# Optimization experiments

Measured on AMD Instinct MI355X. Metric: run time of the kernel, lower is better.

## Reference

```python
import jax, jax.numpy as jnp
import numpy as np

B, D = 500000, 3
EPS = 1e-8

def _matrix_sqrt_H(A):
    # Hermitian sqrt via eigh: Q diag((L^2)^0.25) Q^T  (matches torch code incl. |L| handling)
    L, Q = jnp.linalg.eigh(A)
    return jnp.einsum('bij,bj,bkj->bik', Q, (L ** 2) ** 0.25, Q)

def setup_inputs() -> dict:
    key = jax.random.key(0)
    k1, k2, k3, k4 = jax.random.split(key, 4)
    miu_1 = jax.random.normal(k1, (B, D), dtype=jnp.float32)
    miu_2 = jax.random.normal(k2, (B, D), dtype=jnp.float32)
    eye = jnp.eye(D, dtype=jnp.float32)
    M1 = jax.random.normal(k3, (B, D, D), dtype=jnp.float32)
    M2 = jax.random.normal(k4, (B, D, D), dtype=jnp.float32)
    # SPD covariances, as produced by a Gaussian-splatting pipeline
    cov_1 = 0.1 * jnp.einsum('bij,bkj->bik', M1, M1) + 1e-3 * eye
    cov_2 = 0.1 * jnp.einsum('bij,bkj->bik', M2, M2) + 1e-3 * eye
    return {"miu_1": miu_1, "miu_2": miu_2, "cov_1": cov_1, "cov_2": cov_2}

def reference(miu_1, miu_2, cov_1, cov_2):
    eye = jnp.eye(cov_1.shape[-1], dtype=cov_1.dtype)
    A_sqrt = _matrix_sqrt_H(cov_1 + eye * EPS)
    A_sqrt_inv = jnp.linalg.inv(A_sqrt + eye * EPS)
    C = jnp.einsum('bij,bjk,blk->bil', A_sqrt, cov_2, A_sqrt)  # A_sqrt cov_2 A_sqrt^T
    C_sqrt = _matrix_sqrt_H(C + eye * EPS)
    cov_velocity = jnp.einsum('bij,bjk,blk->bil', A_sqrt, C_sqrt, A_sqrt_inv)
    cov_velocity = cov_velocity + jnp.swapaxes(cov_velocity, -1, -2) - 2.0 * cov_1
    return (miu_2 - miu_1, cov_velocity)
```

## Files before the change

### kernel.cpp

```cpp
#include <hip/hip_runtime.h>
#include <math.h>

#define EPS 1e-8f

__device__ __forceinline__ void jrot(float A[3][3], float Q[3][3], int p, int q, int r) {
    float apq  = A[p][q];
    float diff = A[q][q] - A[p][p];
    float theta = diff * __builtin_amdgcn_rcpf(2.0f * apq);
    float t = __builtin_amdgcn_rcpf(fabsf(theta) + sqrtf(fmaf(theta, theta, 1.0f)));
    t = copysignf(t, theta);
    t = (fabsf(apq) < 1e-30f) ? 0.0f : t;
    float c = __builtin_amdgcn_rsqf(fmaf(t, t, 1.0f));
    float s = t * c;
    float tapq = t * apq;
    A[p][p] -= tapq;
    A[q][q] += tapq;
    A[p][q] = 0.0f; A[q][p] = 0.0f;
    float arp = A[r][p], arq = A[r][q];
    A[r][p] = fmaf(c, arp, -s * arq); A[p][r] = A[r][p];
    A[r][q] = fmaf(c, arq,  s * arp); A[q][r] = A[r][q];
    #pragma unroll
    for (int i = 0; i < 3; ++i) {
        float qip = Q[i][p], qiq = Q[i][q];
        Q[i][p] = fmaf(c, qip, -s * qiq);
        Q[i][q] = fmaf(s, qip,  c * qiq);
    }
}

__device__ __forceinline__ void eigh3f(float A[3][3], float Q[3][3]) {
    Q[0][0] = 1.0f; Q[0][1] = 0.0f; Q[0][2] = 0.0f;
    Q[1][0] = 0.0f; Q[1][1] = 1.0f; Q[1][2] = 0.0f;
    Q[2][0] = 0.0f; Q[2][1] = 0.0f; Q[2][2] = 1.0f;
    #pragma unroll
    for (int sweep = 0; sweep < 5; ++sweep) {
        jrot(A, Q, 0, 1, 2);
        jrot(A, Q, 0, 2, 1);
        jrot(A, Q, 1, 2, 0);
    }
}

__global__ __launch_bounds__(256) void wasserstein_log_kernel(
    const float* __restrict__ miu1, const float* __restrict__ miu2,
    const float* __restrict__ cov1, const float* __restrict__ cov2,
    float* __restrict__ out, int B)
{
    int b = blockIdx.x * blockDim.x + threadIdx.x;
    if (b >= B) return;

    out[3*b + 0] = miu2[3*b + 0] - miu1[3*b + 0];
    out[3*b + 1] = miu2[3*b + 1] - miu1[3*b + 1];
    out[3*b + 2] = miu2[3*b + 2] - miu1[3*b + 2];

    float c1[3][3], c2m[3][3];
    #pragma unroll
    for (int i = 0; i < 3; ++i)
        #pragma unroll
        for (int j = 0; j < 3; ++j) {
            c1[i][j]  = cov1[9*b + 3*i + j];
            c2m[i][j] = cov2[9*b + 3*i + j];
        }

    float A[3][3];
    #pragma unroll
    for (int i = 0; i < 3; ++i)
        #pragma unroll
        for (int j = 0; j < 3; ++j)
            A[i][j] = c1[i][j] + (i == j ? EPS : 0.0f);
    float Q[3][3];
    eigh3f(A, Q);

    float s[3], si[3];
    #pragma unroll
    for (int k = 0; k < 3; ++k) {
        s[k]  = sqrtf(fabsf(A[k][k]));
        si[k] = __builtin_amdgcn_rcpf(s[k] + EPS);
    }

    float S[3][3], Sinv[3][3];
    #pragma unroll
    for (int i = 0; i < 3; ++i)
        #pragma unroll
        for (int j = 0; j < 3; ++j) {
            S[i][j]    = fmaf(Q[i][0]*s[0],  Q[j][0], fmaf(Q[i][1]*s[1],  Q[j][1], Q[i][2]*s[2]  * Q[j][2]));
            Sinv[i][j] = fmaf(Q[i][0]*si[0], Q[j][0], fmaf(Q[i][1]*si[1], Q[j][1], Q[i][2]*si[2] * Q[j][2]));
        }

    float T[3][3];
    #pragma unroll
    for (int i = 0; i < 3; ++i)
        #pragma unroll
        for (int k = 0; k < 3; ++k)
            T[i][k] = fmaf(S[i][0], c2m[0][k], fmaf(S[i][1], c2m[1][k], S[i][2]*c2m[2][k]));
    float C[3][3];
    #pragma unroll
    for (int i = 0; i < 3; ++i)
        #pragma unroll
        for (int l = 0; l < 3; ++l)
            C[i][l] = fmaf(T[i][0], S[l][0], fmaf(T[i][1], S[l][1], T[i][2]*S[l][2]))
                      + (i == l ? EPS : 0.0f);

    float Qc[3][3];
    eigh3f(C, Qc);
    float t0 = sqrtf(fabsf(C[0][0])), t1 = sqrtf(fabsf(C[1][1])), t2 = sqrtf(fabsf(C[2][2]));
    float Csq[3][3];
    #pragma unroll
    for (int i = 0; i < 3; ++i)
        #pragma unroll
        for (int j = 0; j < 3; ++j)
            Csq[i][j] = fmaf(Qc[i][0]*t0, Qc[j][0], fmaf(Qc[i][1]*t1, Qc[j][1], Qc[i][2]*t2 * Qc[j][2]));

    float T2[3][3];
    #pragma unroll
    for (int i = 0; i < 3; ++i)
        #pragma unroll
        for (int k = 0; k < 3; ++k)
            T2[i][k] = fmaf(S[i][0], Csq[0][k], fmaf(S[i][1], Csq[1][k], S[i][2]*Csq[2][k]));
    float V[3][3];
    #pragma unroll
    for (int i = 0; i < 3; ++i)
        #pragma unroll
        for (int l = 0; l < 3; ++l)
            V[i][l] = fmaf(T2[i][0], Sinv[l][0], fmaf(T2[i][1], Sinv[l][1], T2[i][2]*Sinv[l][2]));

    float* out_cov = out + (size_t)3 * B;
    #pragma unroll
    for (int i = 0; i < 3; ++i)
        #pragma unroll
        for (int j = 0; j < 3; ++j)
            out_cov[9*b + 3*i + j] = V[i][j] + V[j][i] - 2.0f*c1[i][j];
}

extern "C" void kernel_launch(void* const* d_in, const int* in_sizes, int n_in,
                              void* d_out, int out_size, void* d_ws, size_t ws_size,
                              hipStream_t stream) {
    const float* miu1 = (const float*)d_in[0];
    const float* miu2 = (const float*)d_in[1];
    const float* cov1 = (const float*)d_in[2];
    const float* cov2 = (const float*)d_in[3];
    float* out = (float*)d_out;
    int B = in_sizes[0] / 3;
    int threads = 256;
    int blocks = (B + threads - 1) / threads;
    hipLaunchKernelGGL(wasserstein_log_kernel, dim3(blocks), dim3(threads), 0, stream,
                       miu1, miu2, cov1, cov2, out, B);
}
```

Baseline: 108.4 us.

## Work in eigenbasis, cheaper Jacobi rotation, fewer sweeps, two items per thread

Several changes at once. The Jacobi rotation now computes c and s from half-angle formulas using rsq and sqrt instead of the tan formulation, and each eigensolve runs 4 sweeps instead of 5. C is formed directly in A's eigenbasis, so the explicit S and Sinv matrices are no longer built, and the final product is fused into U·diag(tsq)·Pᵀ. Each thread now handles two batch elements, which halves the grid. Together these cut ALU work and instruction count, at the cost of slightly lower Jacobi accuracy and higher register pressure.

```diff
diff --git a/kernel.cpp b/kernel.cpp
--- a/kernel.cpp
+++ b/kernel.cpp
@@ -5,13 +5,18 @@
 
 __device__ __forceinline__ void jrot(float A[3][3], float Q[3][3], int p, int q, int r) {
     float apq  = A[p][q];
-    float diff = A[q][q] - A[p][p];
-    float theta = diff * __builtin_amdgcn_rcpf(2.0f * apq);
-    float t = __builtin_amdgcn_rcpf(fabsf(theta) + sqrtf(fmaf(theta, theta, 1.0f)));
-    t = copysignf(t, theta);
-    t = (fabsf(apq) < 1e-30f) ? 0.0f : t;
-    float c = __builtin_amdgcn_rsqf(fmaf(t, t, 1.0f));
-    float s = t * c;
+    float h    = A[q][q] - A[p][p];
+    float ah   = fabsf(h) + 1e-18f;
+    float v    = apq + apq;
+    float rad  = fmaf(ah, ah, v * v);
+    float rr   = __builtin_amdgcn_rsqf(rad);
+    float c2   = ah * rr;
+    float s2h  = apq * rr;
+    s2h = (h < 0.0f) ? -s2h : s2h;
+    float c    = sqrtf(fmaf(0.5f, c2, 0.5f));
+    float rc   = __builtin_amdgcn_rcpf(c);
+    float s    = s2h * rc;
+    float t    = s * rc;
     float tapq = t * apq;
     A[p][p] -= tapq;
     A[q][q] += tapq;
@@ -32,7 +37,7 @@
     Q[1][0] = 0.0f; Q[1][1] = 1.0f; Q[1][2] = 0.0f;
     Q[2][0] = 0.0f; Q[2][1] = 0.0f; Q[2][2] = 1.0f;
     #pragma unroll
-    for (int sweep = 0; sweep < 5; ++sweep) {
+    for (int sweep = 0; sweep < 4; ++sweep) {
         jrot(A, Q, 0, 1, 2);
         jrot(A, Q, 0, 2, 1);
         jrot(A, Q, 1, 2, 0);
@@ -42,92 +47,95 @@
 __global__ __launch_bounds__(256) void wasserstein_log_kernel(
     const float* __restrict__ miu1, const float* __restrict__ miu2,
     const float* __restrict__ cov1, const float* __restrict__ cov2,
-    float* __restrict__ out, int B)
+    float* __restrict__ out, int B, int B2)
 {
-    int b = blockIdx.x * blockDim.x + threadIdx.x;
-    if (b >= B) return;
+    int b0 = blockIdx.x * blockDim.x + threadIdx.x;
+    if (b0 >= B2) return;
+    float* out_cov = out + (size_t)3 * B;
 
-    out[3*b + 0] = miu2[3*b + 0] - miu1[3*b + 0];
-    out[3*b + 1] = miu2[3*b + 1] - miu1[3*b + 1];
-    out[3*b + 2] = miu2[3*b + 2] - miu1[3*b + 2];
+    #pragma unroll
+    for (int e = 0; e < 2; ++e) {
+        int b = b0 + e * B2;
+        if (b >= B) continue;
 
-    float c1[3][3], c2m[3][3];
-    #pragma unroll
-    for (int i = 0; i < 3; ++i)
+        out[3*b + 0] = miu2[3*b + 0] - miu1[3*b + 0];
+        out[3*b + 1] = miu2[3*b + 1] - miu1[3*b + 1];
+        out[3*b + 2] = miu2[3*b + 2] - miu1[3*b + 2];
+
+        float A[3][3], M[3][3];
         #pragma unroll
-        for (int j = 0; j < 3; ++j) {
-            c1[i][j]  = cov1[9*b + 3*i + j];
-            c2m[i][j] = cov2[9*b + 3*i + j];
+        for (int i = 0; i < 3; ++i)
+            #pragma unroll
+            for (int j = 0; j < 3; ++j) {
+                A[i][j] = cov1[9*b + 3*i + j];
+                M[i][j] = cov2[9*b + 3*i + j];
+            }
+        float k00 = A[0][0], k01 = A[0][1], k02 = A[0][2];
+        float k11 = A[1][1], k12 = A[1][2], k22 = A[2][2];
+        A[0][0] += EPS; A[1][1] += EPS; A[2][2] += EPS;
+
+        float Q[3][3];
+        eigh3f(A, Q);
+
+        float d[3], di[3];
+        #pragma unroll
+        for (int k = 0; k < 3; ++k) {
+            float w = fmaxf(fabsf(A[k][k]), 1e-12f);
+            di[k] = __builtin_amdgcn_rsqf(w);
+            d[k]  = w * di[k];
         }
 
-    float A[3][3];
-    #pragma unroll
-    for (int i = 0; i < 3; ++i)
+        float T[3][3];
         #pragma unroll
-        for (int j = 0; j < 3; ++j)
-            A[i][j] = c1[i][j] + (i == j ? EPS : 0.0f);
-    float Q[3][3];
-    eigh3f(A, Q);
+        for (int i = 0; i < 3; ++i)
+            #pragma unroll
+            for (int j = 0; j < 3; ++j)
+                T[i][j] = fmaf(Q[0][i], M[0][j], fmaf(Q[1][i], M[1][j], Q[2][i]*M[2][j]));
+        float Cp[3][3];
+        #pragma unroll
+        for (int i = 0; i < 3; ++i)
+            #pragma unroll
+            for (int j = 0; j < 3; ++j) {
+                float g = fmaf(T[i][0], Q[0][j], fmaf(T[i][1], Q[1][j], T[i][2]*Q[2][j]));
+                Cp[i][j] = d[i] * d[j] * g + (i == j ? EPS : 0.0f);
+            }
 
-    float s[3], si[3];
-    #pragma unroll
-    for (int k = 0; k < 3; ++k) {
-        s[k]  = sqrtf(fabsf(A[k][k]));
-        si[k] = __builtin_amdgcn_rcpf(s[k] + EPS);
-    }
-
-    float S[3][3], Sinv[3][3];
-    #pragma unroll
-    for (int i = 0; i < 3; ++i)
+        float Qc[3][3];
+        eigh3f(Cp, Qc);
+        float tsq[3];
         #pragma unroll
-        for (int j = 0; j < 3; ++j) {
-            S[i][j]    = fmaf(Q[i][0]*s[0],  Q[j][0], fmaf(Q[i][1]*s[1],  Q[j][1], Q[i][2]*s[2]  * Q[j][2]));
-            Sinv[i][j] = fmaf(Q[i][0]*si[0], Q[j][0], fmaf(Q[i][1]*si[1], Q[j][1], Q[i][2]*si[2] * Q[j][2]));
+        for (int k = 0; k < 3; ++k) {
+            float wc = fmaxf(fabsf(Cp[k][k]), 1e-12f);
+            tsq[k] = wc * __builtin_amdgcn_rsqf(wc);
         }
 
-    float T[3][3];
-    #pragma unroll
-    for (int i = 0; i < 3; ++i)
+        float U[3][3], P[3][3];
         #pragma unroll
-        for (int k = 0; k < 3; ++k)
-            T[i][k] = fmaf(S[i][0], c2m[0][k], fmaf(S[i][1], c2m[1][k], S[i][2]*c2m[2][k]));
-    float C[3][3];
-    #pragma unroll
-    for (int i = 0; i < 3; ++i)
+        for (int i = 0; i < 3; ++i)
+            #pragma unroll
+            for (int j = 0; j < 3; ++j) {
+                float q0 = Q[i][0], q1 = Q[i][1], q2 = Q[i][2];
+                U[i][j] = fmaf(q0*d[0],  Qc[0][j], fmaf(q1*d[1],  Qc[1][j], q2*d[2]  * Qc[2][j]));
+                P[i][j] = fmaf(q0*di[0], Qc[0][j], fmaf(q1*di[1], Qc[1][j], q2*di[2] * Qc[2][j]));
+            }
+        float V[3][3];
         #pragma unroll
-        for (int l = 0; l < 3; ++l)
-            C[i][l] = fmaf(T[i][0], S[l][0], fmaf(T[i][1], S[l][1], T[i][2]*S[l][2]))
-                      + (i == l ? EPS : 0.0f);
+        for (int i = 0; i < 3; ++i)
+            #pragma unroll
+            for (int j = 0; j < 3; ++j)
+                V[i][j] = fmaf(U[i][0]*tsq[0], P[j][0],
+                          fmaf(U[i][1]*tsq[1], P[j][1], U[i][2]*tsq[2] * P[j][2]));
 
-    float Qc[3][3];
-    eigh3f(C, Qc);
-    float t0 = sqrtf(fabsf(C[0][0])), t1 = sqrtf(fabsf(C[1][1])), t2 = sqrtf(fabsf(C[2][2]));
-    float Csq[3][3];
-    #pragma unroll
-    for (int i = 0; i < 3; ++i)
-        #pragma unroll
-        for (int j = 0; j < 3; ++j)
-            Csq[i][j] = fmaf(Qc[i][0]*t0, Qc[j][0], fmaf(Qc[i][1]*t1, Qc[j][1], Qc[i][2]*t2 * Qc[j][2]));
-
-    float T2[3][3];
-    #pragma unroll
-    for (int i = 0; i < 3; ++i)
-        #pragma unroll
-        for (int k = 0; k < 3; ++k)
-            T2[i][k] = fmaf(S[i][0], Csq[0][k], fmaf(S[i][1], Csq[1][k], S[i][2]*Csq[2][k]));
-    float V[3][3];
-    #pragma unroll
-    for (int i = 0; i < 3; ++i)
-        #pragma unroll
-        for (int l = 0; l < 3; ++l)
-            V[i][l] = fmaf(T2[i][0], Sinv[l][0], fmaf(T2[i][1], Sinv[l][1], T2[i][2]*Sinv[l][2]));
-
-    float* out_cov = out + (size_t)3 * B;
-    #pragma unroll
-    for (int i = 0; i < 3; ++i)
-        #pragma unroll
-        for (int j = 0; j < 3; ++j)
-            out_cov[9*b + 3*i + j] = V[i][j] + V[j][i] - 2.0f*c1[i][j];
+        out_cov[9*b + 0] = V[0][0] + V[0][0] - 2.0f*k00;
+        out_cov[9*b + 1] = V[0][1] + V[1][0] - 2.0f*k01;
+        out_cov[9*b + 2] = V[0][2] + V[2][0] - 2.0f*k02;
+        out_cov[9*b + 3] = V[1][0] + V[0][1] - 2.0f*k01;
+        out_cov[9*b + 4] = V[1][1] + V[1][1] - 2.0f*k11;
+        out_cov[9*b + 5] = V[1][2] + V[2][1] - 2.0f*k12;
+        out_cov[9*b + 6] = V[2][0] + V[0][2] - 2.0f*k02;
+        out_cov[9*b + 7] = V[2][1] + V[1][2] - 2.0f*k12;
+        out_cov[9*b + 8] = V[2][2] + V[2][2] - 2.0f*k22;
+    }
 }
 
 extern "C" void kernel_launch(void* const* d_in, const int* in_sizes, int n_in,
@@ -138,9 +146,10 @@
     const float* cov1 = (const float*)d_in[2];
     const float* cov2 = (const float*)d_in[3];
     float* out = (float*)d_out;
-    int B = in_sizes[0] / 3;
+    int B  = in_sizes[0] / 3;
+    int B2 = (B + 1) / 2;
     int threads = 256;
-    int blocks = (B + threads - 1) / threads;
+    int blocks = (B2 + threads - 1) / threads;
     hipLaunchKernelGGL(wasserstein_log_kernel, dim3(blocks), dim3(threads), 0, stream,
-                       miu1, miu2, cov1, cov2, out, B);
+                       miu1, miu2, cov1, cov2, out, B, B2);
 }
```

Result: faster. 105.2 us (-3.0%).

## Process two matrices per thread with packed float2 math and reduced Jacobi sweeps

Applied to the files above, without the earlier changes.

Each thread now handles two batch elements packed as float2 vectors, so the compiler can emit packed FP32 instructions. The Jacobi eigensolver is cut from 5 sweeps to one specialised first sweep plus 2 full sweeps, and the rotation angle is computed with a half-angle rsqrt formula. Loads and stores use 16-byte vector accesses, and only the symmetric half of each matrix is read. The algebra is restructured to reuse eigenvectors of A (C formed in the Q basis) and to build the symmetric output directly. Fewer sweeps may lower accuracy on ill-conditioned matrices, and halving the thread count reduces parallelism.

```diff
diff --git a/kernel.cpp b/kernel.cpp
--- a/kernel.cpp
+++ b/kernel.cpp
@@ -3,131 +3,245 @@
 
 #define EPS 1e-8f
 
-__device__ __forceinline__ void jrot(float A[3][3], float Q[3][3], int p, int q, int r) {
-    float apq  = A[p][q];
-    float diff = A[q][q] - A[p][p];
-    float theta = diff * __builtin_amdgcn_rcpf(2.0f * apq);
-    float t = __builtin_amdgcn_rcpf(fabsf(theta) + sqrtf(fmaf(theta, theta, 1.0f)));
-    t = copysignf(t, theta);
-    t = (fabsf(apq) < 1e-30f) ? 0.0f : t;
-    float c = __builtin_amdgcn_rsqf(fmaf(t, t, 1.0f));
-    float s = t * c;
-    float tapq = t * apq;
-    A[p][p] -= tapq;
-    A[q][q] += tapq;
-    A[p][q] = 0.0f; A[q][p] = 0.0f;
-    float arp = A[r][p], arq = A[r][q];
-    A[r][p] = fmaf(c, arp, -s * arq); A[p][r] = A[r][p];
-    A[r][q] = fmaf(c, arq,  s * arp); A[q][r] = A[r][q];
+typedef float v2  __attribute__((ext_vector_type(2)));
+typedef float f4a __attribute__((ext_vector_type(4), aligned(4)));
+
+static __device__ __forceinline__ v2 vfma(v2 a, v2 b, v2 c) {
+#if __has_builtin(__builtin_elementwise_fma)
+    return __builtin_elementwise_fma(a, b, c);
+#else
+    return a * b + c;
+#endif
+}
+static __device__ __forceinline__ v2 vrsq(v2 x) {
+    v2 r; r.x = __builtin_amdgcn_rsqf(x.x); r.y = __builtin_amdgcn_rsqf(x.y); return r;
+}
+static __device__ __forceinline__ v2 vsq(v2 x)         { return __builtin_elementwise_sqrt(x); }
+static __device__ __forceinline__ v2 vab(v2 x)         { return __builtin_elementwise_abs(x); }
+static __device__ __forceinline__ v2 vmx(v2 a, v2 b)   { return __builtin_elementwise_max(a, b); }
+static __device__ __forceinline__ v2 vcs(v2 a, v2 b)   { return __builtin_elementwise_copysign(a, b); }
+
+static __device__ __forceinline__ void jangle(v2 app, v2 aqq, v2 apq,
+                                              v2 &c, v2 &s, v2 &app2, v2 &aqq2) {
+    v2 h   = aqq - app;
+    v2 ah  = vab(h) + 1e-18f;
+    v2 v   = apq + apq;
+    v2 rad = vfma(ah, ah, v * v);
+    v2 rr  = vrsq(rad);
+    v2 c2  = ah * rr;
+    c = vsq(vfma((v2)0.5f, c2, (v2)0.5f));
+    v2 s2 = vmx(vfma((v2)(-0.5f), c2, (v2)0.5f), (v2)0.0f);
+    s = vcs(vsq(s2), apq * h);
+    v2 dl = vcs(vfma(rad, rr, -ah), h) * 0.5f;
+    app2 = app - dl;
+    aqq2 = aqq + dl;
+}
+
+static __device__ __forceinline__ void eigh3(
+    v2 &a00, v2 &a01, v2 &a02, v2 &a11, v2 &a12, v2 &a22,
+    v2 &q00, v2 &q01, v2 &q02, v2 &q10, v2 &q11, v2 &q12, v2 &q20, v2 &q21, v2 &q22)
+{
+    v2 c, s, x, y, t0, t1;
+    jangle(a00, a11, a01, c, s, x, y); a00 = x; a11 = y; a01 = (v2)0.0f;
+    t0 = a02; t1 = a12; a02 = vfma(c, t0, -s * t1); a12 = vfma(c, t1, s * t0);
+    q00 = c; q01 = s; q10 = -s; q11 = c;
+
+    jangle(a00, a22, a02, c, s, x, y); a00 = x; a22 = y; a02 = (v2)0.0f;
+    t0 = a01; t1 = a12; a01 = vfma(c, t0, -s * t1); a12 = vfma(c, t1, s * t0);
+    q02 = s * q00; q12 = s * q10; q20 = -s; q22 = c;
+    q00 = c * q00; q10 = c * q10;
+
+    jangle(a11, a22, a12, c, s, x, y); a11 = x; a22 = y; a12 = (v2)0.0f;
+    t0 = a01; t1 = a02; a01 = vfma(c, t0, -s * t1); a02 = vfma(c, t1, s * t0);
+    t0 = q01; t1 = q02; q01 = vfma(c, t0, -s * t1); q02 = vfma(s, t0, c * t1);
+    t0 = q11; t1 = q12; q11 = vfma(c, t0, -s * t1); q12 = vfma(s, t0, c * t1);
+    q21 = -s * q22; q22 = c * q22;
+
     #pragma unroll
-    for (int i = 0; i < 3; ++i) {
-        float qip = Q[i][p], qiq = Q[i][q];
-        Q[i][p] = fmaf(c, qip, -s * qiq);
-        Q[i][q] = fmaf(s, qip,  c * qiq);
+    for (int sw = 0; sw < 2; ++sw) {
+        jangle(a00, a11, a01, c, s, x, y); a00 = x; a11 = y; a01 = (v2)0.0f;
+        t0 = a02; t1 = a12; a02 = vfma(c, t0, -s * t1); a12 = vfma(c, t1, s * t0);
+        t0 = q00; t1 = q01; q00 = vfma(c, t0, -s * t1); q01 = vfma(s, t0, c * t1);
+        t0 = q10; t1 = q11; q10 = vfma(c, t0, -s * t1); q11 = vfma(s, t0, c * t1);
+        t0 = q20; t1 = q21; q20 = vfma(c, t0, -s * t1); q21 = vfma(s, t0, c * t1);
+
+        jangle(a00, a22, a02, c, s, x, y); a00 = x; a22 = y; a02 = (v2)0.0f;
+        t0 = a01; t1 = a12; a01 = vfma(c, t0, -s * t1); a12 = vfma(c, t1, s * t0);
+        t0 = q00; t1 = q02; q00 = vfma(c, t0, -s * t1); q02 = vfma(s, t0, c * t1);
+        t0 = q10; t1 = q12; q10 = vfma(c, t0, -s * t1); q12 = vfma(s, t0, c * t1);
+        t0 = q20; t1 = q22; q20 = vfma(c, t0, -s * t1); q22 = vfma(s, t0, c * t1);
+
+        jangle(a11, a22, a12, c, s, x, y); a11 = x; a22 = y; a12 = (v2)0.0f;
+        t0 = a01; t1 = a02; a01 = vfma(c, t0, -s * t1); a02 = vfma(c, t1, s * t0);
+        t0 = q01; t1 = q02; q01 = vfma(c, t0, -s * t1); q02 = vfma(s, t0, c * t1);
+        t0 = q11; t1 = q12; q11 = vfma(c, t0, -s * t1); q12 = vfma(s, t0, c * t1);
+        t0 = q21; t1 = q22; q21 = vfma(c, t0, -s * t1); q22 = vfma(s, t0, c * t1);
     }
 }
 
-__device__ __forceinline__ void eigh3f(float A[3][3], float Q[3][3]) {
-    Q[0][0] = 1.0f; Q[0][1] = 0.0f; Q[0][2] = 0.0f;
-    Q[1][0] = 0.0f; Q[1][1] = 1.0f; Q[1][2] = 0.0f;
-    Q[2][0] = 0.0f; Q[2][1] = 0.0f; Q[2][2] = 1.0f;
-    #pragma unroll
-    for (int sweep = 0; sweep < 5; ++sweep) {
-        jrot(A, Q, 0, 1, 2);
-        jrot(A, Q, 0, 2, 1);
-        jrot(A, Q, 1, 2, 0);
-    }
-}
-
-__global__ __launch_bounds__(256) void wasserstein_log_kernel(
+__global__ __launch_bounds__(256, 4) void wasserstein_log_kernel(
     const float* __restrict__ miu1, const float* __restrict__ miu2,
     const float* __restrict__ cov1, const float* __restrict__ cov2,
     float* __restrict__ out, int B)
 {
-    int b = blockIdx.x * blockDim.x + threadIdx.x;
-    if (b >= B) return;
-
-    out[3*b + 0] = miu2[3*b + 0] - miu1[3*b + 0];
-    out[3*b + 1] = miu2[3*b + 1] - miu1[3*b + 1];
-    out[3*b + 2] = miu2[3*b + 2] - miu1[3*b + 2];
-
-    float c1[3][3], c2m[3][3];
-    #pragma unroll
-    for (int i = 0; i < 3; ++i)
-        #pragma unroll
-        for (int j = 0; j < 3; ++j) {
-            c1[i][j]  = cov1[9*b + 3*i + j];
-            c2m[i][j] = cov2[9*b + 3*i + j];
-        }
-
-    float A[3][3];
-    #pragma unroll
-    for (int i = 0; i < 3; ++i)
-        #pragma unroll
-        for (int j = 0; j < 3; ++j)
-            A[i][j] = c1[i][j] + (i == j ? EPS : 0.0f);
-    float Q[3][3];
-    eigh3f(A, Q);
-
-    float s[3], si[3];
-    #pragma unroll
-    for (int k = 0; k < 3; ++k) {
-        s[k]  = sqrtf(fabsf(A[k][k]));
-        si[k] = __builtin_amdgcn_rcpf(s[k] + EPS);
+    int b0 = blockIdx.x * blockDim.x + threadIdx.x;
+    int nT = (B + 1) >> 1;
+    if (b0 >= nT) return;
+    bool pair = (2 * b0 + 1 < B);
+
+    v2 k00, k01, k02, k11, k12, k22;
+    v2 m00, m01, m02, m11, m12, m22;
+    v2 u0, u1, u2;
+
+    if (pair) {
+        size_t cb = 18 * (size_t)b0;
+        const f4a* p1 = (const f4a*)(cov1 + cb);
+        f4a A0 = p1[0], A1 = p1[1], A2 = p1[2], A3 = p1[3];
+        float a17 = cov1[cb + 17];
+        k00.x = A0.x; k00.y = A2.y;
+        k01.x = A0.y; k01.y = A2.z;
+        k02.x = A0.z; k02.y = A2.w;
+        k11.x = A1.x; k11.y = A3.y;
+        k12.x = A1.y; k12.y = A3.z;
+        k22.x = A2.x; k22.y = a17;
+
+        const f4a* p2 = (const f4a*)(cov2 + cb);
+        f4a B0 = p2[0], B1 = p2[1], B2 = p2[2], B3 = p2[3];
+        float b17 = cov2[cb + 17];
+        m00.x = B0.x; m00.y = B2.y;
+        m01.x = B0.y; m01.y = B2.z;
+        m02.x = B0.z; m02.y = B2.w;
+        m11.x = B1.x; m11.y = B3.y;
+        m12.x = B1.y; m12.y = B3.z;
+        m22.x = B2.x; m22.y = b17;
+
+        size_t mb = 6 * (size_t)b0;
+        const f4a* q1 = (const f4a*)(miu1 + mb);
+        const f4a* q2 = (const f4a*)(miu2 + mb);
+        f4a M1 = q1[0]; float m1a = miu1[mb + 4], m1b = miu1[mb + 5];
+        f4a M2 = q2[0]; float m2a = miu2[mb + 4], m2b = miu2[mb + 5];
+        u0.x = M2.x - M1.x; u0.y = M2.w - M1.w;
+        u1.x = M2.y - M1.y; u1.y = m2a - m1a;
+        u2.x = M2.z - M1.z; u2.y = m2b - m1b;
+    } else {
+        size_t cb = 9 * (size_t)(B - 1);
+        k00 = (v2)cov1[cb+0]; k01 = (v2)cov1[cb+1]; k02 = (v2)cov1[cb+2];
+        k11 = (v2)cov1[cb+4]; k12 = (v2)cov1[cb+5]; k22 = (v2)cov1[cb+8];
+        m00 = (v2)cov2[cb+0]; m01 = (v2)cov2[cb+1]; m02 = (v2)cov2[cb+2];
+        m11 = (v2)cov2[cb+4]; m12 = (v2)cov2[cb+5]; m22 = (v2)cov2[cb+8];
+        size_t mb = 3 * (size_t)(B - 1);
+        u0 = (v2)(miu2[mb+0] - miu1[mb+0]);
+        u1 = (v2)(miu2[mb+1] - miu1[mb+1]);
+        u2 = (v2)(miu2[mb+2] - miu1[mb+2]);
     }
 
-    float S[3][3], Sinv[3][3];
-    #pragma unroll
-    for (int i = 0; i < 3; ++i)
-        #pragma unroll
-        for (int j = 0; j < 3; ++j) {
-            S[i][j]    = fmaf(Q[i][0]*s[0],  Q[j][0], fmaf(Q[i][1]*s[1],  Q[j][1], Q[i][2]*s[2]  * Q[j][2]));
-            Sinv[i][j] = fmaf(Q[i][0]*si[0], Q[j][0], fmaf(Q[i][1]*si[1], Q[j][1], Q[i][2]*si[2] * Q[j][2]));
-        }
-
-    float T[3][3];
-    #pragma unroll
-    for (int i = 0; i < 3; ++i)
-        #pragma unroll
-        for (int k = 0; k < 3; ++k)
-            T[i][k] = fmaf(S[i][0], c2m[0][k], fmaf(S[i][1], c2m[1][k], S[i][2]*c2m[2][k]));
-    float C[3][3];
-    #pragma unroll
-    for (int i = 0; i < 3; ++i)
-        #pragma unroll
-        for (int l = 0; l < 3; ++l)
-            C[i][l] = fmaf(T[i][0], S[l][0], fmaf(T[i][1], S[l][1], T[i][2]*S[l][2]))
-                      + (i == l ? EPS : 0.0f);
-
-    float Qc[3][3];
-    eigh3f(C, Qc);
-    float t0 = sqrtf(fabsf(C[0][0])), t1 = sqrtf(fabsf(C[1][1])), t2 = sqrtf(fabsf(C[2][2]));
-    float Csq[3][3];
-    #pragma unroll
-    for (int i = 0; i < 3; ++i)
-        #pragma unroll
-        for (int j = 0; j < 3; ++j)
-            Csq[i][j] = fmaf(Qc[i][0]*t0, Qc[j][0], fmaf(Qc[i][1]*t1, Qc[j][1], Qc[i][2]*t2 * Qc[j][2]));
-
-    float T2[3][3];
-    #pragma unroll
-    for (int i = 0; i < 3; ++i)
-        #pragma unroll
-        for (int k = 0; k < 3; ++k)
-            T2[i][k] = fmaf(S[i][0], Csq[0][k], fmaf(S[i][1], Csq[1][k], S[i][2]*Csq[2][k]));
-    float V[3][3];
-    #pragma unroll
-    for (int i = 0; i < 3; ++i)
-        #pragma unroll
-        for (int l = 0; l < 3; ++l)
-            V[i][l] = fmaf(T2[i][0], Sinv[l][0], fmaf(T2[i][1], Sinv[l][1], T2[i][2]*Sinv[l][2]));
-
-    float* out_cov = out + (size_t)3 * B;
-    #pragma unroll
-    for (int i = 0; i < 3; ++i)
-        #pragma unroll
-        for (int j = 0; j < 3; ++j)
-            out_cov[9*b + 3*i + j] = V[i][j] + V[j][i] - 2.0f*c1[i][j];
+    v2 a00 = k00 + EPS, a01 = k01, a02 = k02,
+       a11 = k11 + EPS, a12 = k12, a22 = k22 + EPS;
+    v2 q00, q01, q02, q10, q11, q12, q20, q21, q22;
+    eigh3(a00, a01, a02, a11, a12, a22,
+          q00, q01, q02, q10, q11, q12, q20, q21, q22);
+
+    v2 w0 = vmx(vab(a00), (v2)1e-12f);
+    v2 w1 = vmx(vab(a11), (v2)1e-12f);
+    v2 w2 = vmx(vab(a22), (v2)1e-12f);
+    v2 di0 = vrsq(w0), di1 = vrsq(w1), di2 = vrsq(w2);
+    v2 d0 = w0 * di0, d1 = w1 * di1, d2 = w2 * di2;
+
+    v2 T00 = vfma(m00, q00, vfma(m01, q10, m02 * q20));
+    v2 T01 = vfma(m00, q01, vfma(m01, q11, m02 * q21));
+    v2 T02 = vfma(m00, q02, vfma(m01, q12, m02 * q22));
+    v2 T10 = vfma(m01, q00, vfma(m11, q10, m12 * q20));
+    v2 T11 = vfma(m01, q01, vfma(m11, q11, m12 * q21));
+    v2 T12 = vfma(m01, q02, vfma(m11, q12, m12 * q22));
+    v2 T20 = vfma(m02, q00, vfma(m12, q10, m22 * q20));
+    v2 T21 = vfma(m02, q01, vfma(m12, q11, m22 * q21));
+    v2 T22 = vfma(m02, q02, vfma(m12, q12, m22 * q22));
+
+    v2 g00 = vfma(q00, T00, vfma(q10, T10, q20 * T20));
+    v2 g01 = vfma(q00, T01, vfma(q10, T11, q20 * T21));
+    v2 g02 = vfma(q00, T02, vfma(q10, T12, q20 * T22));
+    v2 g11 = vfma(q01, T01, vfma(q11, T11, q21 * T21));
+    v2 g12 = vfma(q01, T02, vfma(q11, T12, q21 * T22));
+    v2 g22 = vfma(q02, T02, vfma(q12, T12, q22 * T22));
+
+    v2 cp00 = vfma(w0, g00, (v2)EPS);
+    v2 cp11 = vfma(w1, g11, (v2)EPS);
+    v2 cp22 = vfma(w2, g22, (v2)EPS);
+    v2 cp01 = d0 * d1 * g01;
+    v2 cp02 = d0 * d2 * g02;
+    v2 cp12 = d1 * d2 * g12;
+
+    v2 e00, e01, e02, e10, e11, e12, e20, e21, e22;
+    eigh3(cp00, cp01, cp02, cp11, cp12, cp22,
+          e00, e01, e02, e10, e11, e12, e20, e21, e22);
+    v2 v0 = vmx(vab(cp00), (v2)1e-12f);
+    v2 v1 = vmx(vab(cp11), (v2)1e-12f);
+    v2 v2v = vmx(vab(cp22), (v2)1e-12f);
+    v2 ts0 = v0 * vrsq(v0);
+    v2 ts1 = v1 * vrsq(v1);
+    v2 ts2 = v2v * vrsq(v2v);
+
+    v2 Ed00 = d0*e00, Ed01 = d0*e01, Ed02 = d0*e02;
+    v2 Ed10 = d1*e10, Ed11 = d1*e11, Ed12 = d1*e12;
+    v2 Ed20 = d2*e20, Ed21 = d2*e21, Ed22 = d2*e22;
+    v2 Ei00 = di0*e00, Ei01 = di0*e01, Ei02 = di0*e02;
+    v2 Ei10 = di1*e10, Ei11 = di1*e11, Ei12 = di1*e12;
+    v2 Ei20 = di2*e20, Ei21 = di2*e21, Ei22 = di2*e22;
+
+    v2 U00 = vfma(q00, Ed00, vfma(q01, Ed10, q02 * Ed20));
+    v2 U01 = vfma(q00, Ed01, vfma(q01, Ed11, q02 * Ed21));
+    v2 U02 = vfma(q00, Ed02, vfma(q01, Ed12, q02 * Ed22));
+    v2 U10 = vfma(q10, Ed00, vfma(q11, Ed10, q12 * Ed20));
+    v2 U11 = vfma(q10, Ed01, vfma(q11, Ed11, q12 * Ed21));
+    v2 U12 = vfma(q10, Ed02, vfma(q11, Ed12, q12 * Ed22));
+    v2 U20 = vfma(q20, Ed00, vfma(q21, Ed10, q22 * Ed20));
+    v2 U21 = vfma(q20, Ed01, vfma(q21, Ed11, q22 * Ed21));
+    v2 U22 = vfma(q20, Ed02, vfma(q21, Ed12, q22 * Ed22));
+
+    v2 P00 = vfma(q00, Ei00, vfma(q01, Ei10, q02 * Ei20));
+    v2 P01 = vfma(q00, Ei01, vfma(q01, Ei11, q02 * Ei21));
+    v2 P02 = vfma(q00, Ei02, vfma(q01, Ei12, q02 * Ei22));
+    v2 P10 = vfma(q10, Ei00, vfma(q11, Ei10, q12 * Ei20));
+    v2 P11 = vfma(q10, Ei01, vfma(q11, Ei11, q12 * Ei21));
+    v2 P12 = vfma(q10, Ei02, vfma(q11, Ei12, q12 * Ei22));
+    v2 P20 = vfma(q20, Ei00, vfma(q21, Ei10, q22 * Ei20));
+    v2 P21 = vfma(q20, Ei01, vfma(q21, Ei11, q22 * Ei21));
+    v2 P22 = vfma(q20, Ei02, vfma(q21, Ei12, q22 * Ei22));
+
+    v2 A0v = ts0 * U00, A1v = ts1 * U01, A2v = ts2 * U02;
+    v2 B0v = ts0 * U10, B1v = ts1 * U11, B2v = ts2 * U12;
+    v2 C0v = ts0 * U20, C1v = ts1 * U21, C2v = ts2 * U22;
+
+    v2 W00 = 2.0f * vfma(A0v, P00, vfma(A1v, P01, A2v * P02));
+    v2 W11 = 2.0f * vfma(B0v, P10, vfma(B1v, P11, B2v * P12));
+    v2 W22 = 2.0f * vfma(C0v, P20, vfma(C1v, P21, C2v * P22));
+    v2 W01 = vfma(A0v, P10, vfma(A1v, P11, vfma(A2v, P12,
+             vfma(B0v, P00, vfma(B1v, P01, B2v * P02)))));
+    v2 W02 = vfma(A0v, P20, vfma(A1v, P21, vfma(A2v, P22,
+             vfma(C0v, P00, vfma(C1v, P01, C2v * P02)))));
+    v2 W12 = vfma(B0v, P20, vfma(B1v, P21, vfma(B2v, P22,
+             vfma(C0v, P10, vfma(C1v, P11, C2v * P12)))));
+
+    v2 o00 = vfma((v2)(-2.0f), k00, W00);
+    v2 o01 = vfma((v2)(-2.0f), k01, W01);
+    v2 o02 = vfma((v2)(-2.0f), k02, W02);
+    v2 o11 = vfma((v2)(-2.0f), k11, W11);
+    v2 o12 = vfma((v2)(-2.0f), k12, W12);
+    v2 o22 = vfma((v2)(-2.0f), k22, W22);
+
+    int e0 = 2 * b0;
+    float* om = out + 3 * (size_t)e0;
+    om[0] = u0.x; om[1] = u1.x; om[2] = u2.x;
+    float* oc = out + 3 * (size_t)B + 9 * (size_t)e0;
+    f4a S0; S0.x = o00.x; S0.y = o01.x; S0.z = o02.x; S0.w = o01.x;
+    f4a S1; S1.x = o11.x; S1.y = o12.x; S1.z = o02.x; S1.w = o12.x;
+    ((f4a*)oc)[0] = S0; ((f4a*)oc)[1] = S1; oc[8] = o22.x;
+    if (pair) {
+        om[3] = u0.y; om[4] = u1.y; om[5] = u2.y;
+        f4a S2; S2.x = o00.y; S2.y = o01.y; S2.z = o02.y; S2.w = o01.y;
+        f4a S3; S3.x = o11.y; S3.y = o12.y; S3.z = o02.y; S3.w = o12.y;
+        ((f4a*)(oc + 9))[0] = S2; ((f4a*)(oc + 9))[1] = S3; oc[17] = o22.y;
+    }
 }
 
 extern "C" void kernel_launch(void* const* d_in, const int* in_sizes, int n_in,
@@ -138,9 +252,10 @@
     const float* cov1 = (const float*)d_in[2];
     const float* cov2 = (const float*)d_in[3];
     float* out = (float*)d_out;
-    int B = in_sizes[0] / 3;
+    int B  = in_sizes[0] / 3;
+    int nT = (B + 1) / 2;
     int threads = 256;
-    int blocks = (B + threads - 1) / threads;
+    int blocks = (nT + threads - 1) / threads;
     hipLaunchKernelGGL(wasserstein_log_kernel, dim3(blocks), dim3(threads), 0, stream,
                        miu1, miu2, cov1, cov2, out, B);
 }
```

Measured after the change: 103.3 us. -4.7%, faster.
